# Optimization experiments

Hardware: AMD Instinct MI355X
Metric: run time of the kernel (lower is better)

The kernel has to match this reference:

```python
import jax, jax.numpy as jnp
import numpy as np

N_FACES = 50000
C_IN = 256
C_OUT = 256
K = 9  # kernel_size ** 2
PAD_SIZE = N_FACES + 1


def _pad_features(x, face_is_pad):
    # Faithful to: padded_x = zeros(pad_size, C); padded_x[~face_is_pad] = x
    # rank[i] = position of row i among the non-pad slots (in order)
    rank = jnp.cumsum(~face_is_pad) - 1            # [P]
    rank = jnp.clip(rank, 0, x.shape[0] - 1)
    padded = jnp.where(face_is_pad[:, None], jnp.zeros((), x.dtype), x[rank])
    return padded                                   # [P, C_in]


def setup_inputs() -> dict:
    key = jax.random.key(0)
    k1, k2, k3 = jax.random.split(key, 3)
    x = jax.random.normal(k1, (N_FACES, C_IN), dtype=jnp.float32)
    weight = jax.random.normal(k2, (C_OUT, C_IN, 1, K), dtype=jnp.float32)
    bias = jnp.zeros((C_OUT,), dtype=jnp.float32)
    face_neighborhood = jax.random.randint(k3, (N_FACES, K), 0, PAD_SIZE, dtype=jnp.int64)
    # exactly one pad slot (the last one); sum(~face_is_pad) == N_FACES == x.shape[0]
    face_is_pad = jnp.zeros((PAD_SIZE,), dtype=bool).at[PAD_SIZE - 1].set(True)
    return {"x": x, "weight": weight, "bias": bias,
            "face_neighborhood": face_neighborhood,
            "face_is_pad": face_is_pad, "pad_size": PAD_SIZE}


def reference(x, weight, bias, face_neighborhood, face_is_pad, pad_size):
    # demodulation: per-output-channel L2 normalization of the weight
    dcoefs = jax.lax.rsqrt(jnp.sum(weight * weight, axis=(1, 2, 3)) + 1e-8)  # [O]
    w = weight * dcoefs[:, None, None, None]        # [O, I, 1, K]
    padded = _pad_features(x, face_is_pad)          # [P, I]
    gathered = padded[face_neighborhood]            # [N, K, I]
    # 1x9 conv over gathered neighbors == contraction over (I, K)
    out = jnp.einsum('nki,oik->no', gathered, w[:, :, 0, :]) + bias  # [N, O]
    return out
```

## Files before the change

### kernel.cpp

```cpp
#include <hip/hip_runtime.h>

#define NF    50000
#define PADP  50001
#define KN    9
#define KTOT  2304
#define NCHUNK 782
#define BM3   224
#define NBLK3 224
#define NKT   36
#define ABUF  28672
#define BB    86016
#define IDXO  151552

#define WT_OFF   0u
#define FLAG_OFF 1179648u
#define CNT_OFF  1179904u
#define PADX_OFF 1183744u

typedef float f32x4 __attribute__((ext_vector_type(4)));
typedef __bf16 bf16x8 __attribute__((ext_vector_type(8)));

typedef const __attribute__((address_space(1))) unsigned int* gas_t;
typedef __attribute__((address_space(3))) unsigned int* las_t;

static __device__ __forceinline__ void gll16(const void* g, void* l) {
  __builtin_amdgcn_global_load_lds((gas_t)g, (las_t)l, 16, 0, 0);
}

static __device__ __forceinline__ unsigned short f2bf(float f) {
  unsigned int u = __builtin_bit_cast(unsigned int, f);
  u = u + 0x7fffu + ((u >> 16) & 1u);
  return (unsigned short)(u >> 16);
}


__global__ void k_prep(const float* __restrict__ w, unsigned short* __restrict__ wt,
                       const unsigned char* __restrict__ pad, int* __restrict__ cnt,
                       const unsigned int* __restrict__ raw, int* __restrict__ flag) {
  if (blockIdx.x < 256) {
    int o = blockIdx.x;
    int i = threadIdx.x;
    const float* wr = w + (o * 256 + i) * 9;
    float wv[9];
    float s = 0.f;
#pragma unroll
    for (int k = 0; k < 9; ++k) { wv[k] = wr[k]; s += wv[k] * wv[k]; }
#pragma unroll
    for (int d = 32; d >= 1; d >>= 1) s += __shfl_xor(s, d);
    __shared__ float red[4];
    if ((i & 63) == 0) red[i >> 6] = s;
    __syncthreads();
    float dc = rsqrtf(red[0] + red[1] + red[2] + red[3] + 1e-8f);
#pragma unroll
    for (int k = 0; k < 9; ++k)
      wt[o * KTOT + k * 256 + i] = f2bf(wv[k] * dc);
  } else {
    int cb = blockIdx.x - 256;
    int t = cb * 256 + threadIdx.x;
    bool ip = (t < PADP) ? (pad[t] != 0) : true;
    unsigned long long m = __ballot(ip);
    int c = t >> 6;
    if ((threadIdx.x & 63) == 0 && c < NCHUNK) cnt[c] = __popcll(m);
    if (cb == 0 && threadIdx.x < 64) {
      unsigned int v = raw[threadIdx.x * 2 + 1];
      unsigned long long nz = __ballot(v != 0u);
      if (threadIdx.x == 0) flag[0] = (nz == 0ull) ? 1 : 0;
    }
  }
}

__global__ __launch_bounds__(256) void k_rankpadx(
    const float* __restrict__ x, const unsigned char* __restrict__ pad,
    const int* __restrict__ cnt, unsigned short* __restrict__ padx) {
  const int c = blockIdx.x;
  const int tid = threadIdx.x, w = tid >> 6, lane = tid & 63;
  int s = 0;
  for (int i = tid; i < c; i += 256) s += cnt[i];
#pragma unroll
  for (int d = 32; d >= 1; d >>= 1) s += __shfl_xor(s, d);
  __shared__ int red[4];
  __shared__ int rnk[64];
  if (lane == 0) red[w] = s;
  __syncthreads();
  const int S = red[0] + red[1] + red[2] + red[3];
  if (w == 0) {
    int p = c * 64 + lane;
    bool ip = (p < PADP) ? (pad[p] != 0) : true;
    unsigned long long m = __ballot(ip);
    int before = __popcll(m & ((1ull << lane) - 1ull));
    rnk[lane] = ip ? -1 : (p - (S + before));
  }
  __syncthreads();
  const int col = lane * 4;
#pragma unroll
  for (int i = 0; i < 16; ++i) {
    int rl = i * 4 + w;
    int pp = c * 64 + rl;
    if (pp >= PADP) continue;
    int rr = rnk[rl];
    ushort4 ov;
    if (rr < 0) { ov.x = 0; ov.y = 0; ov.z = 0; ov.w = 0; }
    else {
      const float4 v = *(const float4*)(x + rr * 256 + col);
      ov.x = f2bf(v.x); ov.y = f2bf(v.y); ov.z = f2bf(v.z); ov.w = f2bf(v.w);
    }
    *(ushort4*)(padx + pp * 256 + col) = ov;
  }
}

__global__ __launch_bounds__(512, 1) void k_main(
    const unsigned short* __restrict__ padx,
    const unsigned short* __restrict__ wt,
    const void* __restrict__ nbr,
    const int* __restrict__ flag,
    const float* __restrict__ bias,
    float* __restrict__ out) {
  __shared__ __align__(16) unsigned char sm[159616];
  const int tid = threadIdx.x;
  const int wv = tid >> 6, lane = tid & 63;
  const int m0 = blockIdx.x * BM3;
  int* idxl = (int*)(sm + IDXO);

  const int q = lane & 15, hi = lane >> 4;
  const int wm = wv >> 2, wn = wv & 3;

  float bv[4];
#pragma unroll
  for (int ni = 0; ni < 4; ++ni) bv[ni] = bias[wn * 64 + ni * 16 + q];

  const bool f64 = (flag[0] != 0);
  const long long* n64 = (const long long*)nbr;
  const int* n32 = (const int*)nbr;
  for (int e = tid; e < BM3 * 9; e += 512) {
    int f = m0 + e / 9;
    if (f >= NF) f = NF - 1;
    int k = e - (e / 9) * 9;
    idxl[e] = f64 ? (int)n64[f * KN + k] : n32[f * KN + k];
  }
  __syncthreads();

  const int swsrc = ((tid & 7) ^ ((tid >> 3) & 7)) * 8;
  const int dst16 = tid * 16;
  int rr0 = 0, rr1 = 0, rr2 = 0, rr3 = 0;
  if (tid < 448) {
    rr0 = (tid >> 3);
    rr1 = rr0 + 56; rr2 = rr0 + 112; rr3 = rr0 + 168;
  }
  const int fl0 = tid >> 3;
  const unsigned short* wtb00 = wt + (fl0      ) * KTOT + swsrc;
  const unsigned short* wtb01 = wt + (fl0 +  64) * KTOT + swsrc;
  const unsigned short* wtb10 = wt + (fl0 + 128) * KTOT + swsrc;
  const unsigned short* wtb11 = wt + (fl0 + 192) * KTOT + swsrc;

  const int q7 = q & 7;
  const int s0 = ((hi    ) ^ q7) * 16;
  const int s1 = ((4 + hi) ^ q7) * 16;
  int aoffb[7], bofb[4];
#pragma unroll
  for (int mi = 0; mi < 7; ++mi) aoffb[mi] = (wm * 112 + mi * 16 + q) * 128;
#pragma unroll
  for (int ni = 0; ni < 4; ++ni) bofb[ni] = (wn * 64 + ni * 16 + q) * 128;

  f32x4 acc[7][4];
#pragma unroll
  for (int a = 0; a < 7; ++a)
#pragma unroll
    for (int b = 0; b < 4; ++b) {
      acc[a][b][0] = 0.f; acc[a][b][1] = 0.f; acc[a][b][2] = 0.f; acc[a][b][3] = 0.f;
    }

  int pc0 = 0, pc1 = 0, pc2 = 0, pc3 = 0, pn0 = 0, pn1 = 0, pn2 = 0, pn3 = 0;
  if (tid < 448) {
    pc0 = idxl[rr0 * 9]; pc1 = idxl[rr1 * 9]; pc2 = idxl[rr2 * 9]; pc3 = idxl[rr3 * 9];
    pn0 = pc0; pn1 = pc1; pn2 = pc2; pn3 = pc3;
  }

  if (tid < 448) {
    gll16(padx + pc0 * 256 +  0 + swsrc, sm + dst16);
    gll16(padx + pc1 * 256 +  0 + swsrc, sm + 7168 + dst16);
    gll16(padx + pc2 * 256 +  0 + swsrc, sm + 14336 + dst16);
    gll16(padx + pc3 * 256 +  0 + swsrc, sm + 21504 + dst16);
    gll16(padx + pc0 * 256 + 64 + swsrc, sm + ABUF + dst16);
    gll16(padx + pc1 * 256 + 64 + swsrc, sm + ABUF + 7168 + dst16);
    gll16(padx + pc2 * 256 + 64 + swsrc, sm + ABUF + 14336 + dst16);
    gll16(padx + pc3 * 256 + 64 + swsrc, sm + ABUF + 21504 + dst16);
  }
  gll16(wtb00, sm + BB + dst16);
  gll16(wtb01, sm + BB + 8192 + dst16);
  gll16(wtb10, sm + BB + 16384 + dst16);
  gll16(wtb11, sm + BB + 24576 + dst16);
  asm volatile("s_waitcnt vmcnt(0)" ::: "memory");
  __builtin_amdgcn_s_barrier();

  bf16x8 af[7], bq[4];
  int aC = 0, aN = ABUF, aS = 2 * ABUF;
  int bC = BB, bO = BB + 32768;

#define LD(p) (*(const bf16x8*)(p))
#define SB __builtin_amdgcn_sched_barrier(0);
#define MF(MI) \
  acc[MI][0] = __builtin_amdgcn_mfma_f32_16x16x32_bf16(af[MI], bq[0], acc[MI][0], 0,0,0); \
  acc[MI][1] = __builtin_amdgcn_mfma_f32_16x16x32_bf16(af[MI], bq[1], acc[MI][1], 0,0,0); \
  acc[MI][2] = __builtin_amdgcn_mfma_f32_16x16x32_bf16(af[MI], bq[2], acc[MI][2], 0,0,0); \
  acc[MI][3] = __builtin_amdgcn_mfma_f32_16x16x32_bf16(af[MI], bq[3], acc[MI][3], 0,0,0);
#define TAIL28 \
  SB __builtin_amdgcn_s_barrier(); \
  asm volatile("s_waitcnt lgkmcnt(0)" ::: "memory"); SB \
  __builtin_amdgcn_s_setprio(1); \
  MF(0) MF(1) MF(2) MF(3) MF(4) MF(5) MF(6) \
  __builtin_amdgcn_s_setprio(0); \
  SB __builtin_amdgcn_s_barrier();

#pragma unroll 1
  for (int kt = 0; kt < NKT; ++kt) {
#pragma unroll
    for (int mi = 0; mi < 7; ++mi) af[mi] = LD(sm + aC + aoffb[mi] + s0);
#pragma unroll
    for (int ni = 0; ni < 4; ++ni) bq[ni] = LD(sm + bC + bofb[ni] + s0);
    {
      const int kb = ((kt + 1 < NKT) ? kt + 1 : NKT - 1) * 64;
      gll16(wtb00 + kb, sm + bO + dst16);
      gll16(wtb01 + kb, sm + bO + 8192 + dst16);
      gll16(wtb10 + kb, sm + bO + 16384 + dst16);
      gll16(wtb11 + kb, sm + bO + 24576 + dst16);
    }
    if ((kt & 3) == 1 && tid < 448) {
      int gn = (kt >> 2) + 1; if (gn > 8) gn = 8;
      pn0 = idxl[rr0 * 9 + gn]; pn1 = idxl[rr1 * 9 + gn];
      pn2 = idxl[rr2 * 9 + gn]; pn3 = idxl[rr3 * 9 + gn];
    }
    TAIL28
#pragma unroll
    for (int mi = 0; mi < 7; ++mi) af[mi] = LD(sm + aC + aoffb[mi] + s1);
#pragma unroll
    for (int ni = 0; ni < 4; ++ni) bq[ni] = LD(sm + bC + bofb[ni] + s1);
    SB
    if (tid < 448) {
      const int c0 = ((kt + 2) & 3) * 64;
      const int u0 = ((kt & 3) < 2) ? pc0 : pn0;
      const int u1 = ((kt & 3) < 2) ? pc1 : pn1;
      const int u2 = ((kt & 3) < 2) ? pc2 : pn2;
      const int u3 = ((kt & 3) < 2) ? pc3 : pn3;
      gll16(padx + u0 * 256 + c0 + swsrc, sm + aS + dst16);
      gll16(padx + u1 * 256 + c0 + swsrc, sm + aS + 7168 + dst16);
      gll16(padx + u2 * 256 + c0 + swsrc, sm + aS + 14336 + dst16);
      gll16(padx + u3 * 256 + c0 + swsrc, sm + aS + 21504 + dst16);
      asm volatile("s_waitcnt vmcnt(4)" ::: "memory");
    } else {
      asm volatile("s_waitcnt vmcnt(0)" ::: "memory");
    }
    TAIL28
    { int t0 = aC; aC = aN; aN = aS; aS = t0; }
    { int t1 = bC; bC = bO; bO = t1; }
    if ((kt & 3) == 3) { pc0 = pn0; pc1 = pn1; pc2 = pn2; pc3 = pn3; }
  }
#undef TAIL28
#undef MF
#undef LD
#undef SB
  asm volatile("s_waitcnt vmcnt(0)" ::: "memory");

#pragma unroll
  for (int ni = 0; ni < 4; ++ni) {
    const int col = wn * 64 + ni * 16 + q;
#pragma unroll
    for (int mi = 0; mi < 7; ++mi) {
#pragma unroll
      for (int rr = 0; rr < 4; ++rr) {
        const int row = m0 + wm * 112 + mi * 16 + hi * 4 + rr;
        if (row < NF) out[row * 256 + col] = acc[mi][ni][rr] + bv[ni];
      }
    }
  }
}

extern "C" void kernel_launch(void* const* d_in, const int* in_sizes, int n_in,
                              void* d_out, int out_size, void* d_ws, size_t ws_size,
                              hipStream_t stream) {
  const float* x = (const float*)d_in[0];
  const float* wfull = (const float*)d_in[1];
  const float* bias = (const float*)d_in[2];
  const void* nbr = d_in[3];
  const unsigned char* pad = (const unsigned char*)d_in[4];
  float* out = (float*)d_out;
  char* ws = (char*)d_ws;

  unsigned short* wt   = (unsigned short*)(ws + WT_OFF);
  int* flag            = (int*)(ws + FLAG_OFF);
  int* cnt             = (int*)(ws + CNT_OFF);
  unsigned short* padx = (unsigned short*)(ws + PADX_OFF);

  k_prep<<<452, 256, 0, stream>>>(wfull, wt, pad, cnt, (const unsigned int*)nbr, flag);
  k_rankpadx<<<NCHUNK, 256, 0, stream>>>(x, pad, cnt, padx);
  k_main<<<NBLK3, 512, 0, stream>>>(padx, wt, nbr, flag, bias, out);
}
```

Measured before the change: 85.98 us.

## Cut main-loop barriers to one per K-step and overlap LDS reads with MFMA

The main loop now has a single barrier at the top of each K-step, preceded by a vmcnt wait, in place of the four barriers around the two MFMA halves. Both halves' A/B fragments are read from LDS up front into two register sets. A partial lgkmcnt(11) wait lets the first 28 MFMAs start while the second half's reads are still in flight. The prologue issues weight loads before the second A tile so that vmcnt(4) at loop entry covers the right loads. This trades barrier and wait stalls for about 44 extra VGPRs, with some risk to occupancy or register spills.

```diff
diff --git a/kernel.cpp b/kernel.cpp
--- a/kernel.cpp
+++ b/kernel.cpp
@@ -180,43 +180,46 @@
     gll16(padx + pc1 * 256 +  0 + swsrc, sm + 7168 + dst16);
     gll16(padx + pc2 * 256 +  0 + swsrc, sm + 14336 + dst16);
     gll16(padx + pc3 * 256 +  0 + swsrc, sm + 21504 + dst16);
+  }
+  gll16(wtb00, sm + BB + dst16);
+  gll16(wtb01, sm + BB + 8192 + dst16);
+  gll16(wtb10, sm + BB + 16384 + dst16);
+  gll16(wtb11, sm + BB + 24576 + dst16);
+  if (tid < 448) {
     gll16(padx + pc0 * 256 + 64 + swsrc, sm + ABUF + dst16);
     gll16(padx + pc1 * 256 + 64 + swsrc, sm + ABUF + 7168 + dst16);
     gll16(padx + pc2 * 256 + 64 + swsrc, sm + ABUF + 14336 + dst16);
     gll16(padx + pc3 * 256 + 64 + swsrc, sm + ABUF + 21504 + dst16);
   }
-  gll16(wtb00, sm + BB + dst16);
-  gll16(wtb01, sm + BB + 8192 + dst16);
-  gll16(wtb10, sm + BB + 16384 + dst16);
-  gll16(wtb11, sm + BB + 24576 + dst16);
-  asm volatile("s_waitcnt vmcnt(0)" ::: "memory");
-  __builtin_amdgcn_s_barrier();
-
-  bf16x8 af[7], bq[4];
+
+  bf16x8 af[7], bq[4], af2[7], bq2[4];
   int aC = 0, aN = ABUF, aS = 2 * ABUF;
   int bC = BB, bO = BB + 32768;
 
 #define LD(p) (*(const bf16x8*)(p))
 #define SB __builtin_amdgcn_sched_barrier(0);
-#define MF(MI) \
-  acc[MI][0] = __builtin_amdgcn_mfma_f32_16x16x32_bf16(af[MI], bq[0], acc[MI][0], 0,0,0); \
-  acc[MI][1] = __builtin_amdgcn_mfma_f32_16x16x32_bf16(af[MI], bq[1], acc[MI][1], 0,0,0); \
-  acc[MI][2] = __builtin_amdgcn_mfma_f32_16x16x32_bf16(af[MI], bq[2], acc[MI][2], 0,0,0); \
-  acc[MI][3] = __builtin_amdgcn_mfma_f32_16x16x32_bf16(af[MI], bq[3], acc[MI][3], 0,0,0);
-#define TAIL28 \
-  SB __builtin_amdgcn_s_barrier(); \
-  asm volatile("s_waitcnt lgkmcnt(0)" ::: "memory"); SB \
-  __builtin_amdgcn_s_setprio(1); \
-  MF(0) MF(1) MF(2) MF(3) MF(4) MF(5) MF(6) \
-  __builtin_amdgcn_s_setprio(0); \
-  SB __builtin_amdgcn_s_barrier();
+#define MF(MI, AF, BQ) \
+  acc[MI][0] = __builtin_amdgcn_mfma_f32_16x16x32_bf16(AF[MI], BQ[0], acc[MI][0], 0,0,0); \
+  acc[MI][1] = __builtin_amdgcn_mfma_f32_16x16x32_bf16(AF[MI], BQ[1], acc[MI][1], 0,0,0); \
+  acc[MI][2] = __builtin_amdgcn_mfma_f32_16x16x32_bf16(AF[MI], BQ[2], acc[MI][2], 0,0,0); \
+  acc[MI][3] = __builtin_amdgcn_mfma_f32_16x16x32_bf16(AF[MI], BQ[3], acc[MI][3], 0,0,0);
 
 #pragma unroll 1
   for (int kt = 0; kt < NKT; ++kt) {
+    if (tid < 448) asm volatile("s_waitcnt vmcnt(4)" ::: "memory");
+    else           asm volatile("s_waitcnt vmcnt(0)" ::: "memory");
+    SB
+    __builtin_amdgcn_s_barrier();
+    SB
 #pragma unroll
     for (int mi = 0; mi < 7; ++mi) af[mi] = LD(sm + aC + aoffb[mi] + s0);
 #pragma unroll
     for (int ni = 0; ni < 4; ++ni) bq[ni] = LD(sm + bC + bofb[ni] + s0);
+#pragma unroll
+    for (int mi = 0; mi < 7; ++mi) af2[mi] = LD(sm + aC + aoffb[mi] + s1);
+#pragma unroll
+    for (int ni = 0; ni < 4; ++ni) bq2[ni] = LD(sm + bC + bofb[ni] + s1);
+    SB
     {
       const int kb = ((kt + 1 < NKT) ? kt + 1 : NKT - 1) * 64;
       gll16(wtb00 + kb, sm + bO + dst16);
@@ -224,17 +227,6 @@
       gll16(wtb10 + kb, sm + bO + 16384 + dst16);
       gll16(wtb11 + kb, sm + bO + 24576 + dst16);
     }
-    if ((kt & 3) == 1 && tid < 448) {
-      int gn = (kt >> 2) + 1; if (gn > 8) gn = 8;
-      pn0 = idxl[rr0 * 9 + gn]; pn1 = idxl[rr1 * 9 + gn];
-      pn2 = idxl[rr2 * 9 + gn]; pn3 = idxl[rr3 * 9 + gn];
-    }
-    TAIL28
-#pragma unroll
-    for (int mi = 0; mi < 7; ++mi) af[mi] = LD(sm + aC + aoffb[mi] + s1);
-#pragma unroll
-    for (int ni = 0; ni < 4; ++ni) bq[ni] = LD(sm + bC + bofb[ni] + s1);
-    SB
     if (tid < 448) {
       const int c0 = ((kt + 2) & 3) * 64;
       const int u0 = ((kt & 3) < 2) ? pc0 : pn0;
@@ -245,16 +237,31 @@
       gll16(padx + u1 * 256 + c0 + swsrc, sm + aS + 7168 + dst16);
       gll16(padx + u2 * 256 + c0 + swsrc, sm + aS + 14336 + dst16);
       gll16(padx + u3 * 256 + c0 + swsrc, sm + aS + 21504 + dst16);
-      asm volatile("s_waitcnt vmcnt(4)" ::: "memory");
-    } else {
-      asm volatile("s_waitcnt vmcnt(0)" ::: "memory");
-    }
-    TAIL28
+    }
+    if ((kt & 3) == 1 && tid < 448) {
+      int gn = (kt >> 2) + 1; if (gn > 8) gn = 8;
+      pn0 = idxl[rr0 * 9 + gn]; pn1 = idxl[rr1 * 9 + gn];
+      pn2 = idxl[rr2 * 9 + gn]; pn3 = idxl[rr3 * 9 + gn];
+    }
+    SB
+    asm volatile("s_waitcnt lgkmcnt(11)" ::: "memory");
+    SB
+    __builtin_amdgcn_s_setprio(1);
+    MF(0, af, bq) MF(1, af, bq) MF(2, af, bq) MF(3, af, bq)
+    MF(4, af, bq) MF(5, af, bq) MF(6, af, bq)
+    __builtin_amdgcn_s_setprio(0);
+    SB
+    asm volatile("s_waitcnt lgkmcnt(0)" ::: "memory");
+    SB
+    __builtin_amdgcn_s_setprio(1);
+    MF(0, af2, bq2) MF(1, af2, bq2) MF(2, af2, bq2) MF(3, af2, bq2)
+    MF(4, af2, bq2) MF(5, af2, bq2) MF(6, af2, bq2)
+    __builtin_amdgcn_s_setprio(0);
+    SB
     { int t0 = aC; aC = aN; aN = aS; aS = t0; }
     { int t1 = bC; bC = bO; bO = t1; }
     if ((kt & 3) == 3) { pc0 = pn0; pc1 = pn1; pc2 = pn2; pc3 = pn3; }
   }
-#undef TAIL28
 #undef MF
 #undef LD
 #undef SB
```

After: 85.46 us. About the same (-0.6%).
